# Kernel optimization log

Hardware: AMD Instinct MI355X
Metric: run time of the kernel (lower is better)

The kernel has to match this reference:

```python
import jax, jax.numpy as jnp
import numpy as np

B, CIN, COUT = 16, 32, 64
T, H, W = 20, 32, 32
KT, KH, KW = 3, 3, 3
EPS = 1e-8
SURR_SCALE = 10.0  # SuperSpike surrogate slope


@jax.custom_vjp
def spike(x):
    # forward: heaviside; backward: SuperSpike surrogate gradient
    return (x > 0).astype(x.dtype)

def _spike_fwd(x):
    return (x > 0).astype(x.dtype), x

def _spike_bwd(x, g):
    return (g / (SURR_SCALE * jnp.abs(x) + 1.0) ** 2,)

spike.defvjp(_spike_fwd, _spike_bwd)


def _conv3d(x, w, pad, groups):
    return jax.lax.conv_general_dilated(
        x, w, window_strides=(1, 1, 1),
        padding=[(pad[0], pad[0]), (pad[1], pad[1]), (pad[2], pad[2])],
        rhs_dilation=(1, 1, 1),
        dimension_numbers=('NCDHW', 'OIDHW', 'NCDHW'),
        feature_group_count=groups)


def setup_inputs() -> dict:
    key = jax.random.key(0)
    k0, k1, k2 = jax.random.split(key, 3)
    w_init_mean, w_init_std = 0.05, 0.05
    w_mean = np.sqrt(w_init_mean)
    w_std = np.sqrt(np.sqrt(w_init_mean ** 2 + (w_init_std * np.sqrt(1.0 / (CIN * KT * KH * KW))) ** 2) - w_init_mean)
    x = jax.random.normal(k0, (B, CIN, T, H, W), dtype=jnp.float32)
    w_dw = w_mean + w_std * jax.random.normal(k1, (CIN, 1, KT, KH, KW), dtype=jnp.float32)
    w_pw = w_mean + w_std * jax.random.normal(k2, (COUT, CIN, 1, 1, 1), dtype=jnp.float32)
    beta = jnp.full((1,), 0.9, dtype=jnp.float32)  # one_per_layer, constant init, clamped [0,1]
    b = jnp.ones((COUT,), dtype=jnp.float32)       # constant init 1.0, clamped >= 0
    return {'x': x, 'w_dw': w_dw, 'w_pw': w_pw, 'beta': beta, 'b': b}


def reference(x, w_dw, w_pw, beta, b):
    pad = (1, 1, 1)  # ceil((3-1)*1/2) per dim; same padding also (faithfully) used for the 1x1x1 conv
    conv_x = _conv3d(x, w_dw, pad, CIN)[:, :, :, :H, :W]          # depthwise, crop to input_shape
    conv_x = _conv3d(conv_x, w_pw, pad, 1)[:, :, :, :H, :W]        # pointwise (time grows T -> T+2)
    nb_steps = conv_x.shape[2]

    # effective full kernel = depthwise * pointwise (broadcast over kernel dims)
    w_tmp = jnp.broadcast_to(jnp.transpose(w_dw, (1, 0, 2, 3, 4)), (COUT, CIN, KT, KH, KW)) * w_pw
    d = jnp.einsum('abcde,fbcde->af', w_tmp, w_tmp)                # lateral inhibition matrix [COUT, COUT]
    norm = (w_tmp ** 2).sum((1, 2, 3, 4))                          # [COUT]
    inv_norm = 1.0 / (norm + EPS)

    def step(carry, inp):
        mem, spk = carry
        rst = jnp.einsum('abcd,be->aecd', spk, d)                  # lateral reset
        mem = (mem - rst) * beta + inp * (1.0 - beta)              # leaky soft-reset update
        mthr = mem * inv_norm[None, :, None, None] - b[None, :, None, None]
        spk = spike(mthr)
        return (mem, spk), spk

    conv_t = jnp.moveaxis(conv_x, 2, 0)                            # [nb_steps, B, COUT, H, W]
    zeros = jnp.zeros((B, COUT, H, W), dtype=x.dtype)
    _, spks = jax.lax.scan(step, (zeros, zeros), conv_t)
    spk_rec = jnp.moveaxis(spks, 0, 2)                             # [B, COUT, nb_steps, H, W]

    loss = 0.5 * (spk_rec ** 2).mean()                             # 'squared'
    spk_spread_loss = spk_rec.sum((0, 1, 3, 4)).max() / (B * COUT * H * W)  # 'max'
    return spk_rec, loss, spk_spread_loss
```

## Files before the change

### kernel.cpp

```cpp
#include <hip/hip_runtime.h>

#define BB_   16
#define CIN_  32
#define COUT_ 64
#define TT_   20
#define NSTEP 22
#define NPIX  1024
#define HW_   32

typedef float f32x16 __attribute__((ext_vector_type(16)));

#define N_DWOUT 10485760ULL
#define N_DW2   10485760ULL
#define OFF_DWOUT 0ULL
#define OFF_DW2   (OFF_DWOUT + N_DWOUT)
#define OFF_D     (OFF_DW2 + N_DW2)
#define OFF_INVN  (OFF_D + 4096ULL)
#define OFF_CNT   (OFF_INVN + 64ULL)
#define WS_FLOATS (OFF_CNT + 32ULL)

__global__ __launch_bounds__(128)
void k_depthwise(const float* __restrict__ x, const float* __restrict__ wdw,
                 float* __restrict__ dwout) {
    const int blk = blockIdx.x;
    const int t4 = blk & 3;
    const int ci = (blk >> 2) & 31;
    const int b  = blk >> 7;
    const int tid = threadIdx.x;
    __shared__ float pl[3][34][35];

    float w[27];
#pragma unroll
    for (int k = 0; k < 27; ++k) w[k] = wdw[ci * 27 + k];

    for (int i = tid; i < 3 * 34 * 35; i += 128) (&pl[0][0][0])[i] = 0.f;
    __syncthreads();

    const float* xb = x + (size_t)(b * 32 + ci) * TT_ * NPIX;
    const int lr = tid >> 2;
    const int lc = (tid & 3) * 8;

    auto load_plane = [&](int p, int slot) {
        const float* s = xb + (size_t)p * NPIX + lr * 32 + lc;
        float4 v0 = *(const float4*)s;
        float4 v1 = *(const float4*)(s + 4);
        float* d = &pl[slot][1 + lr][1 + lc];
        d[0] = v0.x; d[1] = v0.y; d[2] = v0.z; d[3] = v0.w;
        d[4] = v1.x; d[5] = v1.y; d[6] = v1.z; d[7] = v1.w;
    };
    auto zero_plane = [&](int slot) {
        float* d = &pl[slot][1 + lr][1 + lc];
#pragma unroll
        for (int j = 0; j < 8; ++j) d[j] = 0.f;
    };

    const int T0 = t4 * 5;
    if (T0 > 0) load_plane(T0 - 1, (T0 - 1) % 3);
    load_plane(T0, T0 % 3);

    const int hd = lr, wd0 = lc;
    const float* base = &pl[0][0][0];

    for (int t = T0; t < T0 + 5; ++t) {
        __syncthreads();
        const int pnext = t + 1;
        if (pnext < TT_) load_plane(pnext, pnext % 3);
        else             zero_plane(pnext % 3);
        __syncthreads();

        const int sm1 = (t + 2) % 3, s0 = t % 3, sp1 = (t + 1) % 3;
        float acc[8] = {0.f,0.f,0.f,0.f,0.f,0.f,0.f,0.f};
#pragma unroll
        for (int kt = 0; kt < 3; ++kt) {
            const int slot = (kt == 0) ? sm1 : (kt == 1) ? s0 : sp1;
            const float* Pp = base + slot * (34 * 35);
#pragma unroll
            for (int kh = 0; kh < 3; ++kh) {
                const float* row = Pp + (hd + kh) * 35 + wd0;
                float r[10];
#pragma unroll
                for (int m = 0; m < 10; ++m) r[m] = row[m];
#pragma unroll
                for (int kw = 0; kw < 3; ++kw) {
                    const float wv = w[(kt * 3 + kh) * 3 + kw];
#pragma unroll
                    for (int j = 0; j < 8; ++j) acc[j] = fmaf(wv, r[j + kw], acc[j]);
                }
            }
        }
        float* dst = dwout + ((size_t)(b * 32 + ci) * TT_ + t) * NPIX + hd * 32 + wd0;
        *(float4*)dst       = make_float4(acc[0], acc[1], acc[2], acc[3]);
        *(float4*)(dst + 4) = make_float4(acc[4], acc[5], acc[6], acc[7]);
    }
}

__global__ __launch_bounds__(256)
void k_dmat(const float* __restrict__ wdw, const float* __restrict__ wpw,
            float* __restrict__ dmat, float* __restrict__ invn,
            unsigned* __restrict__ gcnt) {
    __shared__ double S[32];
    const int tid = threadIdx.x;
    if (tid < NSTEP) gcnt[tid] = 0u;
    if (tid < 32) {
        double s = 0.0;
        for (int k = 0; k < 27; ++k) { double v = (double)wdw[tid * 27 + k]; s += v * v; }
        S[tid] = s;
    }
    __syncthreads();
    for (int e = tid; e < 4096; e += 256) {
        const int a = e >> 6, f = e & 63;
        double acc = 0.0;
        for (int ci = 0; ci < 32; ++ci)
            acc += (double)wpw[a * 32 + ci] * (double)wpw[f * 32 + ci] * S[ci];
        dmat[e] = (float)acc;
        if (a == f) invn[a] = (float)(1.0 / (acc + 1e-8));
    }
}

__global__ __launch_bounds__(256)
void k_transpose(const float* __restrict__ dwout, float* __restrict__ dw2) {
    const int blk = blockIdx.x;
    const int hq = blk & 7;
    const int bt = blk >> 3;
    const int t  = bt % 20;
    const int b  = bt / 20;
    const int tid = threadIdx.x;
    __shared__ float lt[32][33];
    const int wsrc = tid & 31, cg = tid >> 5;

    for (int hh = 0; hh < 4; ++hh) {
        const int h = hq * 4 + hh;
#pragma unroll
        for (int cc = 0; cc < 4; ++cc) {
            const int ci = cc * 8 + cg;
            lt[wsrc][ci] = dwout[((size_t)(b * 32 + ci) * TT_ + t) * NPIX + h * 32 + wsrc];
        }
        __syncthreads();
        float* drow = dw2 + ((size_t)(b * TT_ + t) * 32 + h) * NPIX;
#pragma unroll
        for (int ss = 0; ss < 4; ++ss) {
            const int slot = ss * 8 + cg;
            drow[slot * 32 + wsrc] = (slot == 0) ? 0.f : lt[slot - 1][wsrc];
        }
        __syncthreads();
    }
}

__global__ __launch_bounds__(512)
void k_recur(const float* __restrict__ dw2, const float* __restrict__ wpw,
             const float* __restrict__ dmat, const float* __restrict__ invn_g,
             const float* __restrict__ beta_g, const float* __restrict__ bvec,
             float* __restrict__ out, unsigned* __restrict__ gcnt) {
    const int blk = blockIdx.x;
    const int whalf = blk & 1;
    const int h = (blk >> 1) & 31;
    const int b = blk >> 6;
    const int tid = threadIdx.x;
    const int lane = tid & 63;
    const int co = lane;
    const int wid = __builtin_amdgcn_readfirstlane(tid >> 6);
    const int w0 = whalf * 16 + wid * 2;

    __shared__ float d_lds[4096];
    __shared__ unsigned long long msk[NSTEP][16];

    for (int i = tid; i < 4096; i += 512) d_lds[i] = dmat[i];
    {
        unsigned long long* mp = &msk[0][0];
        for (int i = tid; i < NSTEP * 16; i += 512) mp[i] = 0ull;
    }

    const float beta_v = beta_g[0];
    const float omb = 1.0f - beta_v;
    const float invn = invn_g[co];
    const float bth  = bvec[co];

    float wa[32];
#pragma unroll
    for (int ci = 0; ci < 32; ++ci) wa[ci] = wpw[co * 32 + ci];

    float mem0 = 0.f, mem1 = 0.f;
    unsigned long long m0p = 0ull, m1p = 0ull;

    {
        const int zco = tid >> 3, zw = (tid & 7) * 2;
        *(float2*)(out + ((size_t)(b * 64 + zco) * NSTEP) * NPIX + h * 32 + whalf * 16 + zw)
            = make_float2(0.f, 0.f);
    }

    __syncthreads();

    const int base0 = ((b * TT_) * 32 + (h - 1)) * NPIX + w0 * 32;
    const bool hok = (h >= 1);

    f32x16 A0, A1, A2, A3;
    if (hok) {
        const float* wrow = dw2 + (size_t)base0;
        A0 = *(const f32x16*)(wrow);
        A1 = *(const f32x16*)(wrow + 16);
        A2 = *(const f32x16*)(wrow + 32);
        A3 = *(const f32x16*)(wrow + 48);
    }

    for (int t = 1; t < NSTEP; ++t) {
        float inp0 = 0.f, inp1 = 0.f;
        if (hok && t <= TT_) {
#pragma unroll
            for (int ci = 0; ci < 16; ++ci) {
                inp0 = fmaf(wa[ci], A0[ci], inp0);
                inp1 = fmaf(wa[ci], A2[ci], inp1);
            }
#pragma unroll
            for (int ci = 0; ci < 16; ++ci) {
                inp0 = fmaf(wa[16 + ci], A1[ci], inp0);
                inp1 = fmaf(wa[16 + ci], A3[ci], inp1);
            }
        }
        if (hok && t < TT_) {
            const float* wrow = dw2 + (size_t)base0 + (size_t)t * (32 * NPIX);
            A0 = *(const f32x16*)(wrow);
            A1 = *(const f32x16*)(wrow + 16);
            A2 = *(const f32x16*)(wrow + 32);
            A3 = *(const f32x16*)(wrow + 48);
        }

        float rst0 = 0.f, rst1 = 0.f;
        unsigned long long mm = m0p;
        while (mm) { const int a = __builtin_ctzll(mm); mm &= mm - 1; rst0 += d_lds[a * 64 + co]; }
        mm = m1p;
        while (mm) { const int a = __builtin_ctzll(mm); mm &= mm - 1; rst1 += d_lds[a * 64 + co]; }

        const float u0 = (mem0 - rst0) * beta_v;
        mem0 = u0 + inp0 * omb;
        const bool s0 = (mem0 * invn - bth) > 0.f;
        const float u1 = (mem1 - rst1) * beta_v;
        mem1 = u1 + inp1 * omb;
        const bool s1 = (mem1 * invn - bth) > 0.f;

        m0p = __ballot(s0);
        m1p = __ballot(s1);
        const int wl = wid * 2;
        if (lane == 0) { msk[t][wl] = m0p; msk[t][wl + 1] = m1p; }
    }
    __syncthreads();

    if (tid < NSTEP) {
        unsigned c = 0;
        for (int w = 0; w < 16; ++w) c += (unsigned)__popcll(msk[tid][w]);
        if (c) atomicAdd(&gcnt[tid], c);
    }

    const int wl = tid & 15;
    for (int it = 0; it < 44; ++it) {
        const int r = it * 32 + (tid >> 4);
        const int tt = r >> 6, cc = r & 63;
        const unsigned long long wv = msk[tt][wl];
        const float sv = (float)((wv >> cc) & 1ull);
        out[((size_t)(b * 64 + cc) * NSTEP + tt) * NPIX + h * 32 + whalf * 16 + wl] = sv;
    }
}

__global__ void k_final(const unsigned* __restrict__ gcnt, float* __restrict__ out,
                        int out_size) {
    if (threadIdx.x == 0 && blockIdx.x == 0) {
        unsigned long long tot = 0; unsigned mx = 0;
        for (int t = 0; t < NSTEP; ++t) { const unsigned c = gcnt[t]; tot += c; if (c > mx) mx = c; }
        const long long nspk = (long long)out_size - 2;
        out[out_size - 2] = (float)(0.5 * ((double)tot / (double)nspk));
        out[out_size - 1] = (float)((double)mx / 1048576.0);
    }
}

extern "C" void kernel_launch(void* const* d_in, const int* in_sizes, int n_in,
                              void* d_out, int out_size, void* d_ws, size_t ws_size,
                              hipStream_t stream) {
    const float* x    = (const float*)d_in[0];
    const float* wdw  = (const float*)d_in[1];
    const float* wpw  = (const float*)d_in[2];
    const float* beta = (const float*)d_in[3];
    const float* bvec = (const float*)d_in[4];
    float* out = (float*)d_out;
    float* ws  = (float*)d_ws;

    if (ws_size < WS_FLOATS * sizeof(float)) return;

    float* dwout = ws + OFF_DWOUT;
    float* dw2   = ws + OFF_DW2;
    float* dmat  = ws + OFF_D;
    float* invn  = ws + OFF_INVN;
    unsigned* gcnt = (unsigned*)(ws + OFF_CNT);

    k_dmat     <<<1, 256, 0, stream>>>(wdw, wpw, dmat, invn, gcnt);
    k_depthwise<<<BB_ * CIN_ * 4, 128, 0, stream>>>(x, wdw, dwout);
    k_transpose<<<BB_ * TT_ * 8, 256, 0, stream>>>(dwout, dw2);
    k_recur    <<<BB_ * HW_ * 2, 512, 0, stream>>>(dw2, wpw, dmat, invn, beta, bvec, out, gcnt);
    k_final    <<<1, 64, 0, stream>>>(gcnt, out, out_size);
}
```

Baseline: 89.72 us.

## Fuse depthwise, transpose, recurrence and final reduction into one cooperative kernel

Merges the four-kernel pipeline into a single cooperative kernel of 1024 blocks x 512 threads. Stages are separated by grid.sync instead of kernel boundaries, and the dmat computation is folded into the transpose phase. The goal is to remove launch overheads and inter-kernel gaps. In exchange it needs all 1024 blocks co-resident (checked through occupancy, with the old path kept as a fallback), and grid-wide barriers plus a changed per-thread work shape in the depthwise stage may cost throughput.

```diff
diff --git a/kernel.cpp b/kernel.cpp
--- a/kernel.cpp
+++ b/kernel.cpp
@@ -1,4 +1,7 @@
 #include <hip/hip_runtime.h>
+#include <hip/hip_cooperative_groups.h>
+
+namespace cg = cooperative_groups;
 
 #define BB_   16
 #define CIN_  32
@@ -19,14 +22,285 @@
 #define OFF_CNT   (OFF_INVN + 64ULL)
 #define WS_FLOATS (OFF_CNT + 32ULL)
 
+#define DW_BLOCKS (BB_ * CIN_ * 4)
+
+__global__ __launch_bounds__(512, 8)
+void k_mega(const float* __restrict__ x, const float* __restrict__ wdw,
+            const float* __restrict__ wpw, const float* __restrict__ beta_g,
+            const float* __restrict__ bvec, float* __restrict__ dwout,
+            float* __restrict__ dw2, float* __restrict__ dmat,
+            float* __restrict__ invn_g, unsigned* __restrict__ gcnt,
+            float* __restrict__ out, int out_size) {
+    cg::grid_group grid = cg::this_grid();
+    const int blk = blockIdx.x;
+    const int tid = threadIdx.x;
+    __shared__ __align__(16) char lsd[28560];
+
+    {
+        if (blk == 1023 && tid < NSTEP) gcnt[tid] = 0u;
+
+        const int grp  = tid >> 8;
+        const int gtid = tid & 255;
+        const int tile = blk * 2 + grp;
+        const int t4 = tile & 3;
+        const int ci = (tile >> 2) & 31;
+        const int b  = tile >> 7;
+
+        float* plbase = (float*)lsd + grp * (3 * 34 * 35);
+        for (int i = gtid; i < 3 * 34 * 35; i += 256) plbase[i] = 0.f;
+
+        const int ciu = __builtin_amdgcn_readfirstlane(ci);
+        float w[27];
+#pragma unroll
+        for (int k = 0; k < 27; ++k) w[k] = wdw[ciu * 27 + k];
+        __syncthreads();
+
+        const float* xb = x + (size_t)(b * 32 + ciu) * TT_ * NPIX;
+        const int lr = gtid >> 3;
+        const int lc = (gtid & 7) * 4;
+
+        auto load_plane = [&](int p, int slot) {
+            const float4 v = *(const float4*)(xb + (size_t)p * NPIX + lr * 32 + lc);
+            float* d = plbase + slot * 1190 + (1 + lr) * 35 + 1 + lc;
+            d[0] = v.x; d[1] = v.y; d[2] = v.z; d[3] = v.w;
+        };
+        auto zero_plane = [&](int slot) {
+            float* d = plbase + slot * 1190 + (1 + lr) * 35 + 1 + lc;
+#pragma unroll
+            for (int j = 0; j < 4; ++j) d[j] = 0.f;
+        };
+
+        const int T0 = t4 * 5;
+        if (T0 > 0) load_plane(T0 - 1, (T0 - 1) % 3);
+        load_plane(T0, T0 % 3);
+
+        const int hd = lr, wd0 = lc;
+        for (int t = T0; t < T0 + 5; ++t) {
+            __syncthreads();
+            const int pnext = t + 1;
+            if (pnext < TT_) load_plane(pnext, pnext % 3);
+            else             zero_plane(pnext % 3);
+            __syncthreads();
+
+            const int sm1 = (t + 2) % 3, s0 = t % 3, sp1 = (t + 1) % 3;
+            float acc[4] = {0.f, 0.f, 0.f, 0.f};
+#pragma unroll
+            for (int kt = 0; kt < 3; ++kt) {
+                const int slot = (kt == 0) ? sm1 : (kt == 1) ? s0 : sp1;
+#pragma unroll
+                for (int kh = 0; kh < 3; ++kh) {
+                    const float* row = plbase + slot * 1190 + (hd + kh) * 35 + wd0;
+                    float r[6];
+#pragma unroll
+                    for (int m = 0; m < 6; ++m) r[m] = row[m];
+#pragma unroll
+                    for (int kw = 0; kw < 3; ++kw) {
+                        const float wv = w[(kt * 3 + kh) * 3 + kw];
+#pragma unroll
+                        for (int j = 0; j < 4; ++j) acc[j] = fmaf(wv, r[j + kw], acc[j]);
+                    }
+                }
+            }
+            float* dst = dwout + ((size_t)(b * 32 + ciu) * TT_ + t) * NPIX + hd * 32 + wd0;
+            *(float4*)dst = make_float4(acc[0], acc[1], acc[2], acc[3]);
+        }
+    }
+    grid.sync();
+
+    {
+        float* lt = (float*)lsd;
+        const int wsrc = tid & 31, cg16 = tid >> 5;
+        for (int tile = blk; tile < BB_ * TT_ * 8; tile += 1024) {
+            const int hq = tile & 7;
+            const int bt = tile >> 3;
+            const int t  = bt % TT_;
+            const int b  = bt / TT_;
+            for (int hh = 0; hh < 4; ++hh) {
+                const int h = hq * 4 + hh;
+#pragma unroll
+                for (int cc = 0; cc < 2; ++cc) {
+                    const int ci = cc * 16 + cg16;
+                    lt[wsrc * 33 + ci] =
+                        dwout[((size_t)(b * 32 + ci) * TT_ + t) * NPIX + h * 32 + wsrc];
+                }
+                __syncthreads();
+                float* drow = dw2 + ((size_t)(b * TT_ + t) * 32 + h) * NPIX;
+#pragma unroll
+                for (int ss = 0; ss < 2; ++ss) {
+                    const int slot = ss * 16 + cg16;
+                    drow[slot * 32 + wsrc] = (slot == 0) ? 0.f : lt[(slot - 1) * 33 + wsrc];
+                }
+                __syncthreads();
+            }
+        }
+        if (blk == 1023) {
+            double* S = (double*)(lsd + 8192);
+            if (tid < 32) {
+                double s = 0.0;
+                for (int k = 0; k < 27; ++k) { double v = (double)wdw[tid * 27 + k]; s += v * v; }
+                S[tid] = s;
+            }
+            __syncthreads();
+            for (int e = tid; e < 4096; e += 512) {
+                const int a = e >> 6, f = e & 63;
+                double acc = 0.0;
+                for (int ci = 0; ci < 32; ++ci)
+                    acc += (double)wpw[a * 32 + ci] * (double)wpw[f * 32 + ci] * S[ci];
+                dmat[e] = (float)acc;
+                if (a == f) invn_g[a] = (float)(1.0 / (acc + 1e-8));
+            }
+        }
+    }
+    grid.sync();
+
+    {
+        const int whalf = blk & 1;
+        const int h = (blk >> 1) & 31;
+        const int b = blk >> 6;
+        const int lane = tid & 63;
+        const int co = lane;
+        const int wid = __builtin_amdgcn_readfirstlane(tid >> 6);
+        const int w0 = whalf * 16 + wid * 2;
+
+        float* d_lds = (float*)lsd;
+        unsigned long long (*msk)[16] = (unsigned long long (*)[16])(lsd + 16384);
+
+        for (int i = tid; i < 4096; i += 512) d_lds[i] = dmat[i];
+        {
+            unsigned long long* mp = &msk[0][0];
+            for (int i = tid; i < NSTEP * 16; i += 512) mp[i] = 0ull;
+        }
+
+        const float beta_v = beta_g[0];
+        const float omb = 1.0f - beta_v;
+        const float invn = invn_g[co];
+        const float bth  = bvec[co];
+
+        float wa[32];
+#pragma unroll
+        for (int ci = 0; ci < 32; ++ci) wa[ci] = wpw[co * 32 + ci];
+
+        float mem0 = 0.f, mem1 = 0.f;
+        unsigned long long m0p = 0ull, m1p = 0ull;
+
+        {
+            const int zco = tid >> 3, zw = (tid & 7) * 2;
+            *(float2*)(out + ((size_t)(b * 64 + zco) * NSTEP) * NPIX + h * 32 + whalf * 16 + zw)
+                = make_float2(0.f, 0.f);
+        }
+        __syncthreads();
+
+        const int base0 = ((b * TT_) * 32 + (h - 1)) * NPIX + w0 * 32;
+        const bool hok = (h >= 1);
+
+        f32x16 A0, A1, A2, A3;
+        if (hok) {
+            const float* wrow = dw2 + (size_t)base0;
+            A0 = *(const f32x16*)(wrow);
+            A1 = *(const f32x16*)(wrow + 16);
+            A2 = *(const f32x16*)(wrow + 32);
+            A3 = *(const f32x16*)(wrow + 48);
+        }
+
+        for (int t = 1; t < NSTEP; ++t) {
+            float inp0 = 0.f, inp1 = 0.f;
+            if (hok && t <= TT_) {
+#pragma unroll
+                for (int ci = 0; ci < 16; ++ci) {
+                    inp0 = fmaf(wa[ci], A0[ci], inp0);
+                    inp1 = fmaf(wa[ci], A2[ci], inp1);
+                }
+#pragma unroll
+                for (int ci = 0; ci < 16; ++ci) {
+                    inp0 = fmaf(wa[16 + ci], A1[ci], inp0);
+                    inp1 = fmaf(wa[16 + ci], A3[ci], inp1);
+                }
+            }
+            if (hok && t < TT_) {
+                const float* wrow = dw2 + (size_t)base0 + (size_t)t * (32 * NPIX);
+                A0 = *(const f32x16*)(wrow);
+                A1 = *(const f32x16*)(wrow + 16);
+                A2 = *(const f32x16*)(wrow + 32);
+                A3 = *(const f32x16*)(wrow + 48);
+            }
+
+            float rst0 = 0.f, rst1 = 0.f;
+            unsigned long long mm = m0p;
+            while (mm) { const int a = __builtin_ctzll(mm); mm &= mm - 1; rst0 += d_lds[a * 64 + co]; }
+            mm = m1p;
+            while (mm) { const int a = __builtin_ctzll(mm); mm &= mm - 1; rst1 += d_lds[a * 64 + co]; }
+
+            const float u0 = (mem0 - rst0) * beta_v;
+            mem0 = u0 + inp0 * omb;
+            const bool s0 = (mem0 * invn - bth) > 0.f;
+            const float u1 = (mem1 - rst1) * beta_v;
+            mem1 = u1 + inp1 * omb;
+            const bool s1 = (mem1 * invn - bth) > 0.f;
+
+            m0p = __ballot(s0);
+            m1p = __ballot(s1);
+            const int wl = wid * 2;
+            if (lane == 0) { msk[t][wl] = m0p; msk[t][wl + 1] = m1p; }
+        }
+        __syncthreads();
+
+        if (tid < NSTEP) {
+            unsigned c = 0;
+            for (int w = 0; w < 16; ++w) c += (unsigned)__popcll(msk[tid][w]);
+            if (c) atomicAdd(&gcnt[tid], c);
+        }
+
+        const int wl = tid & 15;
+        for (int it = 0; it < 44; ++it) {
+            const int r = it * 32 + (tid >> 4);
+            const int tt = r >> 6, cc = r & 63;
+            const unsigned long long wv = msk[tt][wl];
+            const float sv = (float)((wv >> cc) & 1ull);
+            out[((size_t)(b * 64 + cc) * NSTEP + tt) * NPIX + h * 32 + whalf * 16 + wl] = sv;
+        }
+    }
+    grid.sync();
+
+    if (blk == 0 && tid == 0) {
+        unsigned long long tot = 0; unsigned mx = 0;
+        for (int t = 0; t < NSTEP; ++t) { const unsigned c = gcnt[t]; tot += c; if (c > mx) mx = c; }
+        const long long nspk = (long long)out_size - 2;
+        out[out_size - 2] = (float)(0.5 * ((double)tot / (double)nspk));
+        out[out_size - 1] = (float)((double)mx / 1048576.0);
+    }
+}
+
 __global__ __launch_bounds__(128)
 void k_depthwise(const float* __restrict__ x, const float* __restrict__ wdw,
-                 float* __restrict__ dwout) {
+                 const float* __restrict__ wpw, float* __restrict__ dwout,
+                 float* __restrict__ dmat, float* __restrict__ invn,
+                 unsigned* __restrict__ gcnt) {
     const int blk = blockIdx.x;
+    const int tid = threadIdx.x;
+
+    if (blk == DW_BLOCKS) {
+        __shared__ double S[32];
+        if (tid < NSTEP) gcnt[tid] = 0u;
+        if (tid < 32) {
+            double s = 0.0;
+            for (int k = 0; k < 27; ++k) { double v = (double)wdw[tid * 27 + k]; s += v * v; }
+            S[tid] = s;
+        }
+        __syncthreads();
+        for (int e = tid; e < 4096; e += 128) {
+            const int a = e >> 6, f = e & 63;
+            double acc = 0.0;
+            for (int ci = 0; ci < 32; ++ci)
+                acc += (double)wpw[a * 32 + ci] * (double)wpw[f * 32 + ci] * S[ci];
+            dmat[e] = (float)acc;
+            if (a == f) invn[a] = (float)(1.0 / (acc + 1e-8));
+        }
+        return;
+    }
+
     const int t4 = blk & 3;
     const int ci = (blk >> 2) & 31;
     const int b  = blk >> 7;
-    const int tid = threadIdx.x;
     __shared__ float pl[3][34][35];
 
     float w[27];
@@ -95,29 +369,6 @@
 }
 
 __global__ __launch_bounds__(256)
-void k_dmat(const float* __restrict__ wdw, const float* __restrict__ wpw,
-            float* __restrict__ dmat, float* __restrict__ invn,
-            unsigned* __restrict__ gcnt) {
-    __shared__ double S[32];
-    const int tid = threadIdx.x;
-    if (tid < NSTEP) gcnt[tid] = 0u;
-    if (tid < 32) {
-        double s = 0.0;
-        for (int k = 0; k < 27; ++k) { double v = (double)wdw[tid * 27 + k]; s += v * v; }
-        S[tid] = s;
-    }
-    __syncthreads();
-    for (int e = tid; e < 4096; e += 256) {
-        const int a = e >> 6, f = e & 63;
-        double acc = 0.0;
-        for (int ci = 0; ci < 32; ++ci)
-            acc += (double)wpw[a * 32 + ci] * (double)wpw[f * 32 + ci] * S[ci];
-        dmat[e] = (float)acc;
-        if (a == f) invn[a] = (float)(1.0 / (acc + 1e-8));
-    }
-}
-
-__global__ __launch_bounds__(256)
 void k_transpose(const float* __restrict__ dwout, float* __restrict__ dw2) {
     const int blk = blockIdx.x;
     const int hq = blk & 7;
@@ -126,20 +377,20 @@
     const int b  = bt / 20;
     const int tid = threadIdx.x;
     __shared__ float lt[32][33];
-    const int wsrc = tid & 31, cg = tid >> 5;
+    const int wsrc = tid & 31, cgi = tid >> 5;
 
     for (int hh = 0; hh < 4; ++hh) {
         const int h = hq * 4 + hh;
 #pragma unroll
         for (int cc = 0; cc < 4; ++cc) {
-            const int ci = cc * 8 + cg;
+            const int ci = cc * 8 + cgi;
             lt[wsrc][ci] = dwout[((size_t)(b * 32 + ci) * TT_ + t) * NPIX + h * 32 + wsrc];
         }
         __syncthreads();
         float* drow = dw2 + ((size_t)(b * TT_ + t) * 32 + h) * NPIX;
 #pragma unroll
         for (int ss = 0; ss < 4; ++ss) {
-            const int slot = ss * 8 + cg;
+            const int slot = ss * 8 + cgi;
             drow[slot * 32 + wsrc] = (slot == 0) ? 0.f : lt[slot - 1][wsrc];
         }
         __syncthreads();
@@ -187,7 +438,6 @@
         *(float2*)(out + ((size_t)(b * 64 + zco) * NSTEP) * NPIX + h * 32 + whalf * 16 + zw)
             = make_float2(0.f, 0.f);
     }
-
     __syncthreads();
 
     const int base0 = ((b * TT_) * 32 + (h - 1)) * NPIX + w0 * 32;
@@ -290,9 +540,21 @@
     float* invn  = ws + OFF_INVN;
     unsigned* gcnt = (unsigned*)(ws + OFF_CNT);
 
-    k_dmat     <<<1, 256, 0, stream>>>(wdw, wpw, dmat, invn, gcnt);
-    k_depthwise<<<BB_ * CIN_ * 4, 128, 0, stream>>>(x, wdw, dwout);
-    k_transpose<<<BB_ * TT_ * 8, 256, 0, stream>>>(dwout, dw2);
-    k_recur    <<<BB_ * HW_ * 2, 512, 0, stream>>>(dw2, wpw, dmat, invn, beta, bvec, out, gcnt);
-    k_final    <<<1, 64, 0, stream>>>(gcnt, out, out_size);
+    int maxb = 0;
+    bool coop = (hipOccupancyMaxActiveBlocksPerMultiprocessor(
+                     &maxb, (const void*)k_mega, 512, 0) == hipSuccess) && (maxb >= 4);
+    if (coop) {
+        void* args[] = {(void*)&x, (void*)&wdw, (void*)&wpw, (void*)&beta, (void*)&bvec,
+                        (void*)&dwout, (void*)&dw2, (void*)&dmat, (void*)&invn,
+                        (void*)&gcnt, (void*)&out, (void*)&out_size};
+        if (hipLaunchCooperativeKernel((const void*)k_mega, dim3(1024), dim3(512),
+                                       args, 0, stream) != hipSuccess)
+            coop = false;
+    }
+    if (!coop) {
+        k_depthwise<<<DW_BLOCKS + 1, 128, 0, stream>>>(x, wdw, wpw, dwout, dmat, invn, gcnt);
+        k_transpose<<<BB_ * TT_ * 8, 256, 0, stream>>>(dwout, dw2);
+        k_recur    <<<BB_ * HW_ * 2, 512, 0, stream>>>(dw2, wpw, dmat, invn, beta, bvec, out, gcnt);
+        k_final    <<<1, 64, 0, stream>>>(gcnt, out, out_size);
+    }
 }
```

Result: slower. 102.4 us (+14.1%).

## Fuse transpose into depthwise kernel and fold dmat/final into other launches

Applied to the files above, without the earlier changes.

The depthwise kernel now writes its output directly in the shifted, transposed layout that the recurrence consumes, staging each plane through shared memory. This removes the separate transpose kernel and its extra global round trip. The dmat computation moves into an extra block of the depthwise launch, and the final loss reduction runs in the last-finishing recurrence block via an atomic counter, cutting the launch count from five to two. In exchange, the recurrence now reads 32 strided float2 values per step instead of four contiguous 16-wide vectors, and correctness depends on the done-counter protocol.

```diff
diff --git a/kernel.cpp b/kernel.cpp
--- a/kernel.cpp
+++ b/kernel.cpp
@@ -8,32 +8,58 @@
 #define NPIX  1024
 #define HW_   32
 
-typedef float f32x16 __attribute__((ext_vector_type(16)));
-
-#define N_DWOUT 10485760ULL
 #define N_DW2   10485760ULL
-#define OFF_DWOUT 0ULL
-#define OFF_DW2   (OFF_DWOUT + N_DWOUT)
+#define OFF_DW2   0ULL
 #define OFF_D     (OFF_DW2 + N_DW2)
 #define OFF_INVN  (OFF_D + 4096ULL)
 #define OFF_CNT   (OFF_INVN + 64ULL)
-#define WS_FLOATS (OFF_CNT + 32ULL)
+#define OFF_DONE  (OFF_CNT + 24ULL)
+#define WS_FLOATS (OFF_DONE + 8ULL)
+
+#define DW_BLOCKS (BB_ * CIN_ * 4)
+#define PS_ (32 * 32 * 32)
 
 __global__ __launch_bounds__(128)
-void k_depthwise(const float* __restrict__ x, const float* __restrict__ wdw,
-                 float* __restrict__ dwout) {
+void k_dw(const float* __restrict__ x, const float* __restrict__ wdw,
+          const float* __restrict__ wpw, float* __restrict__ dw2,
+          float* __restrict__ dmat, float* __restrict__ invn,
+          unsigned* __restrict__ gcnt, unsigned* __restrict__ done) {
     const int blk = blockIdx.x;
+    const int tid = threadIdx.x;
+
+    if (blk == DW_BLOCKS) {
+        __shared__ double S[32];
+        if (tid < NSTEP) gcnt[tid] = 0u;
+        if (tid == NSTEP) *done = 0u;
+        if (tid < 32) {
+            double s = 0.0;
+            for (int k = 0; k < 27; ++k) { double v = (double)wdw[tid * 27 + k]; s += v * v; }
+            S[tid] = s;
+        }
+        __syncthreads();
+        for (int e = tid; e < 4096; e += 128) {
+            const int a = e >> 6, f = e & 63;
+            double acc = 0.0;
+            for (int ci = 0; ci < 32; ++ci)
+                acc += (double)wpw[a * 32 + ci] * (double)wpw[f * 32 + ci] * S[ci];
+            dmat[e] = (float)acc;
+            if (a == f) invn[a] = (float)(1.0 / (acc + 1e-8));
+        }
+        return;
+    }
+
     const int t4 = blk & 3;
     const int ci = (blk >> 2) & 31;
     const int b  = blk >> 7;
-    const int tid = threadIdx.x;
     __shared__ float pl[3][34][35];
+    __shared__ float sbuf[32][34];
 
     float w[27];
 #pragma unroll
     for (int k = 0; k < 27; ++k) w[k] = wdw[ci * 27 + k];
 
     for (int i = tid; i < 3 * 34 * 35; i += 128) (&pl[0][0][0])[i] = 0.f;
+    for (int i = tid; i < 32 * 34; i += 128) (&sbuf[0][0])[i] = 0.f;
     __syncthreads();
 
     const float* xb = x + (size_t)(b * 32 + ci) * TT_ * NPIX;
@@ -53,6 +79,14 @@
 #pragma unroll
         for (int j = 0; j < 8; ++j) d[j] = 0.f;
     };
+    auto store_shifted = [&](int tt) {
+        const float* src = &sbuf[lr][lc];
+        float4 o0 = make_float4(src[0], src[1], src[2], src[3]);
+        float4 o1 = make_float4(src[4], src[5], src[6], src[7]);
+        float* dst = dw2 + (((size_t)(b * TT_ + tt) * 32 + lr) * 32 + ci) * 32 + lc;
+        *(float4*)dst       = o0;
+        *(float4*)(dst + 4) = o1;
+    };
 
     const int T0 = t4 * 5;
     if (T0 > 0) load_plane(T0 - 1, (T0 - 1) % 3);
@@ -66,6 +100,7 @@
         const int pnext = t + 1;
         if (pnext < TT_) load_plane(pnext, pnext % 3);
         else             zero_plane(pnext % 3);
+        if (t > T0) store_shifted(t - 1);
         __syncthreads();
 
         const int sm1 = (t + 2) % 3, s0 = t % 3, sp1 = (t + 1) % 3;
@@ -88,69 +123,19 @@
                 }
             }
         }
-        float* dst = dwout + ((size_t)(b * 32 + ci) * TT_ + t) * NPIX + hd * 32 + wd0;
-        *(float4*)dst       = make_float4(acc[0], acc[1], acc[2], acc[3]);
-        *(float4*)(dst + 4) = make_float4(acc[4], acc[5], acc[6], acc[7]);
-    }
-}
-
-__global__ __launch_bounds__(256)
-void k_dmat(const float* __restrict__ wdw, const float* __restrict__ wpw,
-            float* __restrict__ dmat, float* __restrict__ invn,
-            unsigned* __restrict__ gcnt) {
-    __shared__ double S[32];
-    const int tid = threadIdx.x;
-    if (tid < NSTEP) gcnt[tid] = 0u;
-    if (tid < 32) {
-        double s = 0.0;
-        for (int k = 0; k < 27; ++k) { double v = (double)wdw[tid * 27 + k]; s += v * v; }
-        S[tid] = s;
-    }
-    __syncthreads();
-    for (int e = tid; e < 4096; e += 256) {
-        const int a = e >> 6, f = e & 63;
-        double acc = 0.0;
-        for (int ci = 0; ci < 32; ++ci)
-            acc += (double)wpw[a * 32 + ci] * (double)wpw[f * 32 + ci] * S[ci];
-        dmat[e] = (float)acc;
-        if (a == f) invn[a] = (float)(1.0 / (acc + 1e-8));
-    }
-}
-
-__global__ __launch_bounds__(256)
-void k_transpose(const float* __restrict__ dwout, float* __restrict__ dw2) {
-    const int blk = blockIdx.x;
-    const int hq = blk & 7;
-    const int bt = blk >> 3;
-    const int t  = bt % 20;
-    const int b  = bt / 20;
-    const int tid = threadIdx.x;
-    __shared__ float lt[32][33];
-    const int wsrc = tid & 31, cg = tid >> 5;
-
-    for (int hh = 0; hh < 4; ++hh) {
-        const int h = hq * 4 + hh;
-#pragma unroll
-        for (int cc = 0; cc < 4; ++cc) {
-            const int ci = cc * 8 + cg;
-            lt[wsrc][ci] = dwout[((size_t)(b * 32 + ci) * TT_ + t) * NPIX + h * 32 + wsrc];
-        }
-        __syncthreads();
-        float* drow = dw2 + ((size_t)(b * TT_ + t) * 32 + h) * NPIX;
-#pragma unroll
-        for (int ss = 0; ss < 4; ++ss) {
-            const int slot = ss * 8 + cg;
-            drow[slot * 32 + wsrc] = (slot == 0) ? 0.f : lt[slot - 1][wsrc];
-        }
-        __syncthreads();
-    }
+#pragma unroll
+        for (int j = 0; j < 8; ++j) sbuf[hd][wd0 + 1 + j] = acc[j];
+    }
+    __syncthreads();
+    store_shifted(T0 + 4);
 }
 
 __global__ __launch_bounds__(512)
 void k_recur(const float* __restrict__ dw2, const float* __restrict__ wpw,
              const float* __restrict__ dmat, const float* __restrict__ invn_g,
              const float* __restrict__ beta_g, const float* __restrict__ bvec,
-             float* __restrict__ out, unsigned* __restrict__ gcnt) {
+             float* __restrict__ out, unsigned* __restrict__ gcnt,
+             unsigned* __restrict__ done, int out_size) {
     const int blk = blockIdx.x;
     const int whalf = blk & 1;
     const int h = (blk >> 1) & 31;
@@ -187,41 +172,31 @@
         *(float2*)(out + ((size_t)(b * 64 + zco) * NSTEP) * NPIX + h * 32 + whalf * 16 + zw)
             = make_float2(0.f, 0.f);
     }
-
-    __syncthreads();
-
-    const int base0 = ((b * TT_) * 32 + (h - 1)) * NPIX + w0 * 32;
+    __syncthreads();
+
+    const size_t rbase = ((size_t)(b * TT_) * 32 + (h - 1)) * (32 * 32) + w0;
     const bool hok = (h >= 1);
 
-    f32x16 A0, A1, A2, A3;
+    float2 A[32];
     if (hok) {
-        const float* wrow = dw2 + (size_t)base0;
-        A0 = *(const f32x16*)(wrow);
-        A1 = *(const f32x16*)(wrow + 16);
-        A2 = *(const f32x16*)(wrow + 32);
-        A3 = *(const f32x16*)(wrow + 48);
+        const float* rp = dw2 + rbase;
+#pragma unroll
+        for (int ci = 0; ci < 32; ++ci) A[ci] = *(const float2*)(rp + ci * 32);
     }
 
     for (int t = 1; t < NSTEP; ++t) {
         float inp0 = 0.f, inp1 = 0.f;
         if (hok && t <= TT_) {
 #pragma unroll
-            for (int ci = 0; ci < 16; ++ci) {
-                inp0 = fmaf(wa[ci], A0[ci], inp0);
-                inp1 = fmaf(wa[ci], A2[ci], inp1);
+            for (int ci = 0; ci < 32; ++ci) {
+                inp0 = fmaf(wa[ci], A[ci].x, inp0);
+                inp1 = fmaf(wa[ci], A[ci].y, inp1);
             }
-#pragma unroll
-            for (int ci = 0; ci < 16; ++ci) {
-                inp0 = fmaf(wa[16 + ci], A1[ci], inp0);
-                inp1 = fmaf(wa[16 + ci], A3[ci], inp1);
-            }
         }
         if (hok && t < TT_) {
-            const float* wrow = dw2 + (size_t)base0 + (size_t)t * (32 * NPIX);
-            A0 = *(const f32x16*)(wrow);
-            A1 = *(const f32x16*)(wrow + 16);
-            A2 = *(const f32x16*)(wrow + 32);
-            A3 = *(const f32x16*)(wrow + 48);
+            const float* rp = dw2 + rbase + (size_t)t * PS_;
+#pragma unroll
+            for (int ci = 0; ci < 32; ++ci) A[ci] = *(const float2*)(rp + ci * 32);
         }
 
         float rst0 = 0.f, rst1 = 0.f;
@@ -258,16 +233,22 @@
         const float sv = (float)((wv >> cc) & 1ull);
         out[((size_t)(b * 64 + cc) * NSTEP + tt) * NPIX + h * 32 + whalf * 16 + wl] = sv;
     }
-}
-
-__global__ void k_final(const unsigned* __restrict__ gcnt, float* __restrict__ out,
-                        int out_size) {
-    if (threadIdx.x == 0 && blockIdx.x == 0) {
-        unsigned long long tot = 0; unsigned mx = 0;
-        for (int t = 0; t < NSTEP; ++t) { const unsigned c = gcnt[t]; tot += c; if (c > mx) mx = c; }
-        const long long nspk = (long long)out_size - 2;
-        out[out_size - 2] = (float)(0.5 * ((double)tot / (double)nspk));
-        out[out_size - 1] = (float)((double)mx / 1048576.0);
+
+    __syncthreads();
+    if (tid == 0) {
+        __threadfence();
+        const unsigned old = atomicAdd(done, 1u);
+        if (old == (BB_ * HW_ * 2) - 1) {
+            unsigned long long tot = 0; unsigned mx = 0;
+            for (int t = 0; t < NSTEP; ++t) {
+                const unsigned c = atomicAdd(&gcnt[t], 0u);
+                tot += c; if (c > mx) mx = c;
+            }
+            const long long nspk = (long long)out_size - 2;
+            out[out_size - 2] = (float)(0.5 * ((double)tot / (double)nspk));
+            out[out_size - 1] = (float)((double)mx / 1048576.0);
+            atomicExch(done, 0u);
+        }
     }
 }
 
@@ -284,15 +265,13 @@
 
     if (ws_size < WS_FLOATS * sizeof(float)) return;
 
-    float* dwout = ws + OFF_DWOUT;
     float* dw2   = ws + OFF_DW2;
     float* dmat  = ws + OFF_D;
     float* invn  = ws + OFF_INVN;
     unsigned* gcnt = (unsigned*)(ws + OFF_CNT);
-
-    k_dmat     <<<1, 256, 0, stream>>>(wdw, wpw, dmat, invn, gcnt);
-    k_depthwise<<<BB_ * CIN_ * 4, 128, 0, stream>>>(x, wdw, dwout);
-    k_transpose<<<BB_ * TT_ * 8, 256, 0, stream>>>(dwout, dw2);
-    k_recur    <<<BB_ * HW_ * 2, 512, 0, stream>>>(dw2, wpw, dmat, invn, beta, bvec, out, gcnt);
-    k_final    <<<1, 64, 0, stream>>>(gcnt, out, out_size);
+    unsigned* done = (unsigned*)(ws + OFF_DONE);
+
+    k_dw   <<<DW_BLOCKS + 1, 128, 0, stream>>>(x, wdw, wpw, dw2, dmat, invn, gcnt, done);
+    k_recur<<<BB_ * HW_ * 2, 512, 0, stream>>>(dw2, wpw, dmat, invn, beta, bvec, out,
+                                               gcnt, done, out_size);
 }
```

Result: slower. 166.8 us (+85.9%).
